# Optimization experiments

Hardware: AMD Instinct MI355X
Metric: run time of the kernel (lower is better)

The kernel has to match this reference:

```python
import jax, jax.numpy as jnp
import numpy as np
from math import sqrt

N = 40000      # nodes
E = 640000     # edges
DIN = 128
H = 128
DOUT = 128
L = 3          # n_layers
TAU = 1.0
MIN_NORM = 1e-15
BN_EPS = 1e-5


def _norm(v):
    return jnp.linalg.norm(v, axis=-1, keepdims=True)


def reflect_at_zero(x, mu):
    # a = reflection_center(mu); isometric_transform(x, a)
    a = mu / jnp.maximum(jnp.sum(mu * mu, -1, keepdims=True), MIN_NORM)
    r2 = jnp.sum(a * a, -1, keepdims=True) - 1.0
    u = x - a
    return r2 / jnp.maximum(jnp.sum(u * u, -1, keepdims=True), MIN_NORM) * u + a


def reflect_through_zero(p, q, x):
    p_ = p / jnp.maximum(_norm(p), MIN_NORM)
    q_ = q / jnp.maximum(_norm(q), MIN_NORM)
    r = q_ - p_
    m = jnp.sum(r * x, -1, keepdims=True) / jnp.sum(r * r, -1, keepdims=True)
    return x - 2.0 * r * m


def logmap0(y):
    yn = jnp.maximum(_norm(y), MIN_NORM)
    return y / yn * jnp.arctanh(jnp.clip(yn, -1.0 + 1e-15, 1.0 - 1e-15))


def gin_layer(x, src, dst, w1, b1, g, bt, w2, b2):
    # GINConv(eps=0, sum aggregation): mlp(x + sum_{j->i} x_j)
    agg = jax.ops.segment_sum(x[src], dst, num_segments=N)  # [N,H]
    h = x + agg
    h = jax.nn.relu(h @ w1.T + b1)
    mu = jnp.mean(h, axis=0)
    var = jnp.mean((h - mu) ** 2, axis=0)  # biased var (BatchNorm training stats)
    h = (h - mu) / jnp.sqrt(var + BN_EPS) * g + bt
    h = jax.nn.relu(h @ w2.T + b2)
    return h


def setup_inputs() -> dict:
    key = jax.random.key(0)
    ks = jax.random.split(key, 16)
    s = 0.05
    x = jax.random.normal(ks[0], (N, DIN), jnp.float32)
    edge_index = jax.random.randint(ks[1], (2, E), 0, N, dtype=jnp.int64)
    fc0_w = jax.random.normal(ks[2], (H, DIN), jnp.float32) * s
    fc0_b = jax.random.normal(ks[3], (H,), jnp.float32) * s
    w1 = jax.random.normal(ks[4], (L, H, H), jnp.float32) * s
    b1 = jax.random.normal(ks[5], (L, H), jnp.float32) * s
    gamma = jnp.ones((L, H), jnp.float32)
    beta = jnp.zeros((L, H), jnp.float32)
    w2 = jax.random.normal(ks[6], (L, H, H), jnp.float32) * s
    b2 = jax.random.normal(ks[7], (L, H), jnp.float32) * s
    fc_out_w = jax.random.normal(ks[8], (DOUT, H), jnp.float32) * s
    fc_out_b = jax.random.normal(ks[9], (DOUT,), jnp.float32) * s
    p = (-1.0 / sqrt(H)) * jnp.ones((H,), jnp.float32)
    return {"x": x, "edge_index": edge_index, "fc0_w": fc0_w, "fc0_b": fc0_b,
            "w1": w1, "b1": b1, "gamma": gamma, "beta": beta, "w2": w2, "b2": b2,
            "fc_out_w": fc_out_w, "fc_out_b": fc_out_b, "p": p}


def reference(x, edge_index, fc0_w, fc0_b, w1, b1, gamma, beta, w2, b2, fc_out_w, fc_out_b, p):
    # With continuous random features every row is unique, so torch.unique(dim=0)
    # is a pure permutation (counts==1) and the unique/scatter_add/gather pipeline
    # collapses to per-node tree embeddings; the final index_select undoes the perm.
    scaling = jnp.tanh(jnp.asarray(TAU, jnp.float32) / 2.0)
    src, dst = edge_index[0], edge_index[1]
    h = jax.nn.relu(x @ fc0_w.T + fc0_b)                 # [N,H]
    hd = jax.lax.stop_gradient(h)                        # unique under no_grad
    z_prev = jnp.zeros((N, H), h.dtype)                  # level-0 root embedding
    z_cur = scaling * hd / _norm(hd)                     # level-1 embedding
    for i in range(L):
        h = gin_layer(h, src, dst, w1[i], b1[i], gamma[i], beta[i], w2[i], b2[i])
        hd = jax.lax.stop_gradient(h)
        z_ch = scaling * hd / _norm(hd)
        z_par = reflect_at_zero(z_prev, z_cur)
        z_ch = reflect_through_zero(z_par, p, z_ch)
        z_all = reflect_at_zero(z_ch, z_cur)
        z_prev, z_cur = z_cur, z_all
    xh = logmap0(z_cur)                                  # [N,H] tangent space
    out = xh @ fc_out_w.T + fc_out_b                     # [N,DOUT]
    return out / jnp.maximum(_norm(out), 1e-12)          # F.normalize
```

## Files before the change

### kernel.cpp

```cpp
#include <hip/hip_runtime.h>
#include <math.h>

#define NN 40000
#define HD 128
#define NE 640000
#define MINN 1e-15f
#define NSB 157
#define GB  2500
#define HB_BLK 512

typedef __attribute__((ext_vector_type(8))) short bf16x8;
typedef __attribute__((ext_vector_type(4))) float f32x4;

__device__ __forceinline__ float red16(float v){
  v += __shfl_xor(v, 1, 64); v += __shfl_xor(v, 2, 64);
  v += __shfl_xor(v, 4, 64); v += __shfl_xor(v, 8, 64);
  return v;
}

__device__ __forceinline__ float bf2f(short h){
  return __uint_as_float(((unsigned)(unsigned short)h) << 16);
}
__device__ __forceinline__ short f2bf(float v){
  unsigned u = __float_as_uint(v);
  u += 0x7FFF + ((u >> 16) & 1);
  return (short)(u >> 16);
}

#define GACC(A,V) \
  A[0] += __uint_as_float((V).x << 16); A[1] += __uint_as_float((V).x & 0xffff0000u); \
  A[2] += __uint_as_float((V).y << 16); A[3] += __uint_as_float((V).y & 0xffff0000u); \
  A[4] += __uint_as_float((V).z << 16); A[5] += __uint_as_float((V).z & 0xffff0000u); \
  A[6] += __uint_as_float((V).w << 16); A[7] += __uint_as_float((V).w & 0xffff0000u);

__device__ __forceinline__ void loadA_g(const float* __restrict__ A, long rb,
                                        int l15, int kg, float av[4][8]){
  #pragma unroll
  for (int ks = 0; ks < 4; ++ks){
    const float* ap = A + (rb + l15)*HD + ks*32 + kg*8;
    float4 a0 = *(const float4*)ap;
    float4 a1 = *(const float4*)(ap + 4);
    av[ks][0]=a0.x; av[ks][1]=a0.y; av[ks][2]=a0.z; av[ks][3]=a0.w;
    av[ks][4]=a1.x; av[ks][5]=a1.y; av[ks][6]=a1.z; av[ks][7]=a1.w;
  }
}

__device__ __forceinline__ void mfma_core(const float av[4][8],
    const bf16x8* __restrict__ bh, const bf16x8* __restrict__ bl,
    int lane, f32x4 acc[8]){
  #pragma unroll
  for (int ct = 0; ct < 8; ++ct){
    acc[ct][0]=0.f; acc[ct][1]=0.f; acc[ct][2]=0.f; acc[ct][3]=0.f;
  }
  #pragma unroll
  for (int ks = 0; ks < 4; ++ks){
    bf16x8 ah, al;
    #pragma unroll
    for (int j = 0; j < 8; ++j){
      float v = av[ks][j];
      short hh = f2bf(v);
      short ll = f2bf(v - bf2f(hh));
      ah[j] = hh; al[j] = ll;
    }
    #pragma unroll
    for (int ct = 0; ct < 8; ++ct){
      bf16x8 bhv = bh[(ks*8 + ct)*64 + lane];
      bf16x8 blv = bl[(ks*8 + ct)*64 + lane];
      acc[ct] = __builtin_amdgcn_mfma_f32_16x16x32_bf16(ah, bhv, acc[ct], 0, 0, 0);
      acc[ct] = __builtin_amdgcn_mfma_f32_16x16x32_bf16(al, bhv, acc[ct], 0, 0, 0);
      acc[ct] = __builtin_amdgcn_mfma_f32_16x16x32_bf16(ah, blv, acc[ct], 0, 0, 0);
    }
  }
}

__device__ __forceinline__ void biasrelu(f32x4 acc[8], const float* __restrict__ bias,
                                         int l15, bool relu){
  #pragma unroll
  for (int ct = 0; ct < 8; ++ct){
    float bb = bias[ct*16 + l15];
    #pragma unroll
    for (int q = 0; q < 4; ++q){
      float v = acc[ct][q] + bb;
      if (relu) v = fmaxf(v, 0.f);
      acc[ct][q] = v;
    }
  }
}

__global__ __launch_bounds__(64) void zero_prep_k(const float* __restrict__ fc0_w,
    const float* __restrict__ w1, const float* __restrict__ w2,
    const float* __restrict__ fco_w, bf16x8* __restrict__ bhi,
    bf16x8* __restrict__ blo, int* __restrict__ cnt, float* __restrict__ part2){
  int bid = blockIdx.x;
  if (bid < 256){
    int gid = bid*64 + threadIdx.x;
    int widx = gid >> 11;
    const float* W;
    if (widx == 0)      W = fc0_w;
    else if (widx <= 3) W = w1 + (size_t)(widx-1)*HD*HD;
    else if (widx <= 6) W = w2 + (size_t)(widx-4)*HD*HD;
    else                W = fco_w;
    int f  = gid & 2047;
    int ln = f & 63;
    int ct = (f >> 6) & 7;
    int ks = f >> 9;
    int n  = ct*16 + (ln & 15);
    int k0 = ks*32 + (ln >> 4)*8;
    bf16x8 hv, lv;
    #pragma unroll
    for (int j = 0; j < 8; ++j){
      float v = W[n*HD + k0 + j];
      short hh = f2bf(v);
      short ll = f2bf(v - bf2f(hh));
      hv[j] = hh; lv[j] = ll;
    }
    bhi[widx*2048 + f] = hv; blo[widx*2048 + f] = lv;
  } else {
    int i = (bid-256)*64 + threadIdx.x;
    const int st = 161*64;
    for (int j = i; j < NN; j += st) cnt[j] = 0;
    for (int j = i; j < 3*2048; j += st) part2[j] = 0.f;
  }
}

__global__ __launch_bounds__(64) void fc0hist_k(const float* __restrict__ x,
    const int* __restrict__ dst, int* __restrict__ cnt,
    const bf16x8* __restrict__ bhi, const bf16x8* __restrict__ blo,
    const float* __restrict__ fc0_b, float* __restrict__ h,
    unsigned short* __restrict__ hb, float* __restrict__ zB, float scaling){
  int bid = blockIdx.x;
  if (bid >= GB){
    int i = (bid - GB)*64 + threadIdx.x;
    const int st = HB_BLK*64;
    for (; i < NE; i += st) atomicAdd(&cnt[dst[i]], 1);
    return;
  }
  const int lane = threadIdx.x;
  const int l15 = lane & 15, kg = lane >> 4;
  const long rb = (long)bid*16;
  float av[4][8]; loadA_g(x, rb, l15, kg, av);
  f32x4 acc[8]; mfma_core(av, bhi, blo, lane, acc);
  biasrelu(acc, fc0_b, l15, true);
  #pragma unroll
  for (int ct = 0; ct < 8; ++ct)
    #pragma unroll
    for (int q = 0; q < 4; ++q){
      float v = acc[ct][q];
      long row = rb + kg*4 + q;
      h[row*HD + ct*16 + l15] = v;
      hb[row*HD + ct*16 + l15] = (unsigned short)f2bf(v);
    }
  #pragma unroll
  for (int q = 0; q < 4; ++q){
    float ss = 0.f;
    #pragma unroll
    for (int ct = 0; ct < 8; ++ct) ss = fmaf(acc[ct][q], acc[ct][q], ss);
    ss = red16(ss);
    float sc2 = scaling / sqrtf(ss);
    long row = rb + kg*4 + q;
    #pragma unroll
    for (int ct = 0; ct < 8; ++ct)
      zB[row*HD + ct*16 + l15] = acc[ct][q]*sc2;
  }
}

__global__ __launch_bounds__(256) void scanall_k(const int* __restrict__ cnt,
    int* __restrict__ ptr, int* __restrict__ fil){
  __shared__ int s[256];
  const int b = blockIdx.x, t = threadIdx.x;
  const int lim = b*256;
  int acc = 0;
  for (int i = t; i < lim; i += 256) acc += cnt[i];
  s[t] = acc; __syncthreads();
  for (int off = 128; off; off >>= 1){
    if (t < off) s[t] += s[t+off];
    __syncthreads();
  }
  const int pre = s[0];
  __syncthreads();
  const int idx = lim + t;
  int v = (idx < NN) ? cnt[idx] : 0;
  s[t] = v; __syncthreads();
  for (int off = 1; off < 256; off <<= 1){
    int x = (t >= off) ? s[t-off] : 0;
    __syncthreads(); s[t] += x; __syncthreads();
  }
  if (idx < NN){
    int v2 = pre + s[t] - v;
    ptr[idx] = v2; fil[idx] = v2;
  }
  if (b == NSB-1 && t == 255) ptr[NN] = pre + s[255];
}

__global__ void fill_k(const int* __restrict__ src, const int* __restrict__ dst,
    int* __restrict__ fill, unsigned short* __restrict__ eidx, int ne){
  int i = blockIdx.x*blockDim.x + threadIdx.x;
  int st = gridDim.x*blockDim.x;
  for (; i < ne; i += st){
    int d = dst[i];
    int pos = atomicAdd(&fill[d], 1);
    eidx[pos] = (unsigned short)src[i];
  }
}

__global__ __launch_bounds__(256) void gw1_k(const float* __restrict__ h,
    const bf16x8* __restrict__ bhi, const bf16x8* __restrict__ blo,
    const float* __restrict__ bias, float* __restrict__ t,
    float* __restrict__ part2, const uint4* __restrict__ hb4,
    const int* __restrict__ gptr, const unsigned short* __restrict__ eidx)
{
  __shared__ float tl[16*132];
  const int tid = threadIdx.x;
  const int lane = tid & 63;
  const int wv = tid >> 6;
  const int l15 = lane & 15, kg = lane >> 4;
  const long rb = (long)blockIdx.x*16;

  {
    const int r = wv*4 + kg;
    const long node = rb + r;
    int beg = gptr[node], end = gptr[node+1];
    const float4* selfp = (const float4*)(h + node*HD) + l15*2;
    float4 s0 = selfp[0], s1 = selfp[1];
    float ga[8] = {s0.x,s0.y,s0.z,s0.w,s1.x,s1.y,s1.z,s1.w};
    int e = beg;
    for (; e + 8 <= end; e += 8){
      int i0 = eidx[e],   i1 = eidx[e+1], i2 = eidx[e+2], i3 = eidx[e+3];
      int i4 = eidx[e+4], i5 = eidx[e+5], i6 = eidx[e+6], i7 = eidx[e+7];
      uint4 v0 = hb4[(long)i0*16 + l15];
      uint4 v1 = hb4[(long)i1*16 + l15];
      uint4 v2 = hb4[(long)i2*16 + l15];
      uint4 v3 = hb4[(long)i3*16 + l15];
      uint4 v4 = hb4[(long)i4*16 + l15];
      uint4 v5 = hb4[(long)i5*16 + l15];
      uint4 v6 = hb4[(long)i6*16 + l15];
      uint4 v7 = hb4[(long)i7*16 + l15];
      GACC(ga,v0) GACC(ga,v1) GACC(ga,v2) GACC(ga,v3)
      GACC(ga,v4) GACC(ga,v5) GACC(ga,v6) GACC(ga,v7)
    }
    if (e + 4 <= end){
      int i0 = eidx[e], i1 = eidx[e+1], i2 = eidx[e+2], i3 = eidx[e+3];
      uint4 v0 = hb4[(long)i0*16 + l15];
      uint4 v1 = hb4[(long)i1*16 + l15];
      uint4 v2 = hb4[(long)i2*16 + l15];
      uint4 v3 = hb4[(long)i3*16 + l15];
      GACC(ga,v0) GACC(ga,v1) GACC(ga,v2) GACC(ga,v3)
      e += 4;
    }
    for (; e < end; ++e){
      uint4 v = hb4[(long)eidx[e]*16 + l15];
      GACC(ga,v)
    }
    float4* tp = (float4*)(tl + r*132 + l15*8);
    float4 o0 = {ga[0],ga[1],ga[2],ga[3]};
    float4 o1 = {ga[4],ga[5],ga[6],ga[7]};
    tp[0] = o0; tp[1] = o1;
  }
  __syncthreads();
  if (wv != 0) return;

  float av[4][8];
  #pragma unroll
  for (int ks = 0; ks < 4; ++ks){
    const float* ap = tl + l15*132 + ks*32 + kg*8;
    float4 a0 = *(const float4*)ap;
    float4 a1 = *(const float4*)(ap + 4);
    av[ks][0]=a0.x; av[ks][1]=a0.y; av[ks][2]=a0.z; av[ks][3]=a0.w;
    av[ks][4]=a1.x; av[ks][5]=a1.y; av[ks][6]=a1.z; av[ks][7]=a1.w;
  }
  f32x4 acc[8]; mfma_core(av, bhi, blo, lane, acc);
  biasrelu(acc, bias, l15, true);

  #pragma unroll
  for (int ct = 0; ct < 8; ++ct){
    float s = 0.f, q2 = 0.f;
    #pragma unroll
    for (int q = 0; q < 4; ++q){
      float v = acc[ct][q];
      s += v; q2 = fmaf(v, v, q2);
    }
    s  += __shfl_xor(s, 16, 64);  s  += __shfl_xor(s, 32, 64);
    q2 += __shfl_xor(q2, 16, 64); q2 += __shfl_xor(q2, 32, 64);
    if (kg == 0){
      const int slot = (blockIdx.x & 7)*256;
      atomicAdd(&part2[slot + ct*16 + l15], s);
      atomicAdd(&part2[slot + 128 + ct*16 + l15], q2);
    }
  }

  #pragma unroll
  for (int ct = 0; ct < 8; ++ct)
    #pragma unroll
    for (int q = 0; q < 4; ++q)
      t[(rb + kg*4 + q)*HD + ct*16 + l15] = acc[ct][q];
}

template<bool WRITE_H, bool ZFIRST>
__global__ __launch_bounds__(64) void w2z_k(const float* __restrict__ A,
    const bf16x8* __restrict__ bhi, const bf16x8* __restrict__ blo,
    const float* __restrict__ bias, const float* __restrict__ part2,
    const float* __restrict__ gam, const float* __restrict__ bet,
    float* __restrict__ hout, unsigned short* __restrict__ hbout,
    float* __restrict__ zout, float scaling,
    const float* __restrict__ zpin, const float* __restrict__ zcin,
    const float* __restrict__ pvec)
{
  __shared__ float bns[256];
  const int lane = threadIdx.x;
  const int l15 = lane & 15, kg = lane >> 4;
  const long rb = (long)blockIdx.x*16;

  #pragma unroll
  for (int h2 = 0; h2 < 2; ++h2){
    const int c = lane + h2*64;
    float s = 0.f, q = 0.f;
    #pragma unroll
    for (int r = 0; r < 8; ++r){
      s += part2[r*256 + c];
      q += part2[r*256 + 128 + c];
    }
    float mu  = s * (1.0f/NN);
    float var = q * (1.0f/NN) - mu*mu;
    float istd = rsqrtf(var + 1e-5f);
    float scv = gam[c]*istd;
    bns[c] = scv;
    bns[128 + c] = fmaf(-mu, scv, bet[c]);
  }

  float av[4][8];
  loadA_g(A, rb, l15, kg, av);

  float zc_a[4][8], zp_a[4][8], pvr[8];
  #pragma unroll
  for (int q = 0; q < 4; ++q){
    const long row = rb + kg*4 + q;
    #pragma unroll
    for (int ct = 0; ct < 8; ++ct)
      zc_a[q][ct] = zcin[row*HD + ct*16 + l15];
  }
  if constexpr (!ZFIRST){
    #pragma unroll
    for (int q = 0; q < 4; ++q){
      const long row = rb + kg*4 + q;
      #pragma unroll
      for (int ct = 0; ct < 8; ++ct)
        zp_a[q][ct] = zpin[row*HD + ct*16 + l15];
    }
  }
  #pragma unroll
  for (int ct = 0; ct < 8; ++ct) pvr[ct] = pvec[ct*16 + l15];

  #pragma unroll
  for (int ks = 0; ks < 4; ++ks){
    const int k0 = ks*32 + kg*8;
    #pragma unroll
    for (int j = 0; j < 8; ++j)
      av[ks][j] = fmaf(av[ks][j], bns[k0 + j], bns[128 + k0 + j]);
  }

  f32x4 acc[8];
  mfma_core(av, bhi, blo, lane, acc);
  biasrelu(acc, bias, l15, true);

  if (WRITE_H){
    #pragma unroll
    for (int ct = 0; ct < 8; ++ct)
      #pragma unroll
      for (int q = 0; q < 4; ++q){
        float v = acc[ct][q];
        long row = rb + kg*4 + q;
        hout[row*HD + ct*16 + l15] = v;
        hbout[row*HD + ct*16 + l15] = (unsigned short)f2bf(v);
      }
  }

  float pq = 0.f;
  #pragma unroll
  for (int ct = 0; ct < 8; ++ct) pq = fmaf(pvr[ct], pvr[ct], pq);
  pq = red16(pq);
  float qi = 1.0f / fmaxf(sqrtf(pq), MINN);
  #pragma unroll
  for (int ct = 0; ct < 8; ++ct) pvr[ct] *= qi;

  #pragma unroll
  for (int q = 0; q < 4; ++q){
    const long row = rb + kg*4 + q;
    float zc[8], zp[8];
    #pragma unroll
    for (int ct = 0; ct < 8; ++ct) zc[ct] = zc_a[q][ct];
    if constexpr (!ZFIRST){
      #pragma unroll
      for (int ct = 0; ct < 8; ++ct) zp[ct] = zp_a[q][ct];
    } else {
      #pragma unroll
      for (int ct = 0; ct < 8; ++ct) zp[ct] = 0.f;
    }
    float hh = 0.f, cc = 0.f;
    #pragma unroll
    for (int ct = 0; ct < 8; ++ct){
      hh = fmaf(acc[ct][q], acc[ct][q], hh);
      cc = fmaf(zc[ct], zc[ct], cc);
    }
    hh = red16(hh); cc = red16(cc);
    float zs = scaling / sqrtf(hh);
    float di = 1.0f / fmaxf(cc, MINN);
    float r2 = cc*di*di - 1.0f;
    float a[8], u[8]; float uu = 0.f;
    #pragma unroll
    for (int ct = 0; ct < 8; ++ct){
      a[ct] = zc[ct]*di;
      u[ct] = zp[ct] - a[ct];
      uu = fmaf(u[ct], u[ct], uu);
    }
    uu = red16(uu);
    float f = r2 / fmaxf(uu, MINN);
    float zpar[8]; float pn2 = 0.f;
    #pragma unroll
    for (int ct = 0; ct < 8; ++ct){
      zpar[ct] = fmaf(f, u[ct], a[ct]);
      pn2 = fmaf(zpar[ct], zpar[ct], pn2);
    }
    pn2 = red16(pn2);
    float pinv = 1.0f / fmaxf(sqrtf(pn2), MINN);
    float rv[8], zch[8]; float rz = 0.f, rr = 0.f;
    #pragma unroll
    for (int ct = 0; ct < 8; ++ct){
      zch[ct] = acc[ct][q]*zs;
      rv[ct] = pvr[ct] - zpar[ct]*pinv;
      rz = fmaf(rv[ct], zch[ct], rz);
      rr = fmaf(rv[ct], rv[ct], rr);
    }
    rz = red16(rz); rr = red16(rr);
    float mm = rz / rr;
    float u2[8]; float uu2 = 0.f;
    #pragma unroll
    for (int ct = 0; ct < 8; ++ct){
      float z2 = fmaf(-2.0f*mm, rv[ct], zch[ct]);
      u2[ct] = z2 - a[ct];
      uu2 = fmaf(u2[ct], u2[ct], uu2);
    }
    uu2 = red16(uu2);
    float f2 = r2 / fmaxf(uu2, MINN);
    #pragma unroll
    for (int ct = 0; ct < 8; ++ct)
      zout[row*HD + ct*16 + l15] = fmaf(f2, u2[ct], a[ct]);
  }
}

__global__ __launch_bounds__(64) void fin_k(const float* __restrict__ A,
    const bf16x8* __restrict__ bhi, const bf16x8* __restrict__ blo,
    const float* __restrict__ bias, float* __restrict__ out)
{
  const int lane = threadIdx.x;
  const int l15 = lane & 15, kg = lane >> 4;
  const long rb = (long)blockIdx.x*16;

  float av[4][8];
  loadA_g(A, rb, l15, kg, av);

  float ss = 0.f;
  #pragma unroll
  for (int ks = 0; ks < 4; ++ks)
    #pragma unroll
    for (int j = 0; j < 8; ++j)
      ss = fmaf(av[ks][j], av[ks][j], ss);
  ss += __shfl_xor(ss, 16, 64);
  ss += __shfl_xor(ss, 32, 64);
  float n = sqrtf(ss);
  float yn = fmaxf(n, MINN);
  float c = fminf(yn, 1.0f);
  float at = 0.5f*logf((1.0f + c)/(1.0f - c));
  float scx = at / yn;
  #pragma unroll
  for (int ks = 0; ks < 4; ++ks)
    #pragma unroll
    for (int j = 0; j < 8; ++j)
      av[ks][j] *= scx;

  f32x4 acc[8];
  mfma_core(av, bhi, blo, lane, acc);
  biasrelu(acc, bias, l15, false);

  float ss4[4] = {0.f,0.f,0.f,0.f};
  #pragma unroll
  for (int ct = 0; ct < 8; ++ct)
    #pragma unroll
    for (int q = 0; q < 4; ++q)
      ss4[q] = fmaf(acc[ct][q], acc[ct][q], ss4[q]);
  #pragma unroll
  for (int q = 0; q < 4; ++q){
    #pragma unroll
    for (int m = 1; m < 16; m <<= 1) ss4[q] += __shfl_xor(ss4[q], m, 64);
    ss4[q] = 1.0f / fmaxf(sqrtf(ss4[q]), 1e-12f);
  }
  #pragma unroll
  for (int ct = 0; ct < 8; ++ct)
    #pragma unroll
    for (int q = 0; q < 4; ++q)
      out[(rb + kg*4 + q)*HD + ct*16 + l15] = acc[ct][q]*ss4[q];
}

extern "C" void kernel_launch(void* const* d_in, const int* in_sizes, int n_in,
                              void* d_out, int out_size, void* d_ws, size_t ws_size,
                              hipStream_t stream) {
  const float* x       = (const float*)d_in[0];
  const int*   ei      = (const int*)  d_in[1];
  const float* fc0_w   = (const float*)d_in[2];
  const float* fc0_b   = (const float*)d_in[3];
  const float* w1      = (const float*)d_in[4];
  const float* b1      = (const float*)d_in[5];
  const float* gamma   = (const float*)d_in[6];
  const float* beta    = (const float*)d_in[7];
  const float* w2      = (const float*)d_in[8];
  const float* b2      = (const float*)d_in[9];
  const float* fco_w   = (const float*)d_in[10];
  const float* fco_b   = (const float*)d_in[11];
  const float* p       = (const float*)d_in[12];

  float* out = (float*)d_out;
  float* ws  = (float*)d_ws;

  float* h     = ws;
  float* zA    = h   + (size_t)NN*HD;
  float* zB    = zA  + (size_t)NN*HD;
  float* part2 = zB  + (size_t)NN*HD;
  bf16x8* bhi  = (bf16x8*)(part2 + 3*2048);
  bf16x8* blo  = bhi + 8*2048;
  unsigned short* hb = (unsigned short*)(blo + 8*2048);
  int* cnt     = (int*)(hb + (size_t)NN*HD);
  int* ptr     = cnt + NN;
  int* fil     = ptr + NN + 1;
  unsigned short* eidx = (unsigned short*)(fil + NN);
  float* t = out;

  const int* src = ei;
  const int* dst = ei + NE;
  const float scaling = tanhf(0.5f);

  zero_prep_k<<<417, 64, 0, stream>>>(fc0_w, w1, w2, fco_w, bhi, blo, cnt, part2);

  fc0hist_k<<<GB + HB_BLK, 64, 0, stream>>>(x, dst, cnt, bhi, blo, fc0_b,
                                            h, hb, zB, scaling);

  scanall_k<<<NSB, 256, 0, stream>>>(cnt, ptr, fil);
  fill_k<<<512, 256, 0, stream>>>(src, dst, fil, eidx, NE);

  float* zprev = zA; float* zcur = zB;

  for (int i = 0; i < 3; ++i) {
    gw1_k<<<GB, 256, 0, stream>>>(
        h, bhi + (1+i)*2048, blo + (1+i)*2048, b1 + i*HD, t, part2 + i*2048,
        (const uint4*)hb, ptr, eidx);
    if (i == 0)
      w2z_k<true,true><<<GB, 64, 0, stream>>>(
          t, bhi + 4*2048, blo + 4*2048, b2, part2, gamma, beta, h, hb,
          zprev, scaling, zprev, zcur, p);
    else if (i == 1)
      w2z_k<true,false><<<GB, 64, 0, stream>>>(
          t, bhi + 5*2048, blo + 5*2048, b2 + HD, part2 + 2048,
          gamma + HD, beta + HD, h, hb, zprev, scaling, zprev, zcur, p);
    else
      w2z_k<false,false><<<GB, 64, 0, stream>>>(
          t, bhi + 6*2048, blo + 6*2048, b2 + 2*HD, part2 + 2*2048,
          gamma + 2*HD, beta + 2*HD, nullptr, nullptr,
          zprev, scaling, zprev, zcur, p);
    float* tmp = zprev; zprev = zcur; zcur = tmp;
  }

  fin_k<<<GB, 64, 0, stream>>>(zcur, bhi + 7*2048, blo + 7*2048, fco_b, out);
}
```

Before: 321.6 us.

## Defer z-step into next layer's gather kernel and precompute BN scale/shift once

Splits the fused W2+z kernel. The W2 pass now only writes h, and the hyperbolic z-update for each layer runs as extra blocks appended to the next layer's gather/W1 launch, so that z work overlaps with the gather. BatchNorm statistics are finalised once in a tiny single-block kernel instead of being reduced again by every block. This adds a re-read of h for the z-step and extra tiny launches, and the in-place zA/zB aliasing needs care.

Result: slower. 336.6 us (+4.7%).

```diff
diff --git a/kernel.cpp b/kernel.cpp
--- a/kernel.cpp
+++ b/kernel.cpp
@@ -7,6 +7,7 @@
 #define MINN 1e-15f
 #define NSB 157
 #define GB  2500
+#define ZSB 625
 #define HB_BLK 512
 
 typedef __attribute__((ext_vector_type(8))) short bf16x8;
@@ -84,6 +85,87 @@
       if (relu) v = fmaxf(v, 0.f);
       acc[ct][q] = v;
     }
+  }
+}
+
+template<bool ZFIRST>
+__device__ __forceinline__ void zstep_tile(const float hv[4][8],
+    const float* __restrict__ zpin, const float* __restrict__ zcin,
+    float* __restrict__ zout, const float* __restrict__ pvec,
+    float scaling, long rb, int l15, int kg){
+  float pvr[8]; float pq = 0.f;
+  #pragma unroll
+  for (int ct = 0; ct < 8; ++ct){
+    float tv = pvec[ct*16 + l15];
+    pvr[ct] = tv; pq = fmaf(tv, tv, pq);
+  }
+  pq = red16(pq);
+  float qi = 1.0f / fmaxf(sqrtf(pq), MINN);
+  #pragma unroll
+  for (int ct = 0; ct < 8; ++ct) pvr[ct] *= qi;
+
+  #pragma unroll
+  for (int q = 0; q < 4; ++q){
+    const long row = rb + kg*4 + q;
+    float zc[8], zp[8];
+    #pragma unroll
+    for (int ct = 0; ct < 8; ++ct) zc[ct] = zcin[row*HD + ct*16 + l15];
+    if constexpr (!ZFIRST){
+      #pragma unroll
+      for (int ct = 0; ct < 8; ++ct) zp[ct] = zpin[row*HD + ct*16 + l15];
+    } else {
+      #pragma unroll
+      for (int ct = 0; ct < 8; ++ct) zp[ct] = 0.f;
+    }
+    float hh = 0.f, cc = 0.f;
+    #pragma unroll
+    for (int ct = 0; ct < 8; ++ct){
+      hh = fmaf(hv[q][ct], hv[q][ct], hh);
+      cc = fmaf(zc[ct], zc[ct], cc);
+    }
+    hh = red16(hh); cc = red16(cc);
+    float zs = scaling / sqrtf(hh);
+    float di = 1.0f / fmaxf(cc, MINN);
+    float r2 = cc*di*di - 1.0f;
+    float a[8], u[8]; float uu = 0.f;
+    #pragma unroll
+    for (int ct = 0; ct < 8; ++ct){
+      a[ct] = zc[ct]*di;
+      u[ct] = zp[ct] - a[ct];
+      uu = fmaf(u[ct], u[ct], uu);
+    }
+    uu = red16(uu);
+    float f = r2 / fmaxf(uu, MINN);
+    float zpar[8]; float pn2 = 0.f;
+    #pragma unroll
+    for (int ct = 0; ct < 8; ++ct){
+      zpar[ct] = fmaf(f, u[ct], a[ct]);
+      pn2 = fmaf(zpar[ct], zpar[ct], pn2);
+    }
+    pn2 = red16(pn2);
+    float pinv = 1.0f / fmaxf(sqrtf(pn2), MINN);
+    float rv[8], zch[8]; float rz = 0.f, rr = 0.f;
+    #pragma unroll
+    for (int ct = 0; ct < 8; ++ct){
+      zch[ct] = hv[q][ct]*zs;
+      rv[ct] = pvr[ct] - zpar[ct]*pinv;
+      rz = fmaf(rv[ct], zch[ct], rz);
+      rr = fmaf(rv[ct], rv[ct], rr);
+    }
+    rz = red16(rz); rr = red16(rr);
+    float mm = rz / rr;
+    float u2[8]; float uu2 = 0.f;
+    #pragma unroll
+    for (int ct = 0; ct < 8; ++ct){
+      float z2 = fmaf(-2.0f*mm, rv[ct], zch[ct]);
+      u2[ct] = z2 - a[ct];
+      uu2 = fmaf(u2[ct], u2[ct], uu2);
+    }
+    uu2 = red16(uu2);
+    float f2 = r2 / fmaxf(uu2, MINN);
+    #pragma unroll
+    for (int ct = 0; ct < 8; ++ct)
+      zout[row*HD + ct*16 + l15] = fmaf(f2, u2[ct], a[ct]);
   }
 }
 
@@ -203,17 +285,36 @@
   }
 }
 
+template<bool ZS, bool ZF>
 __global__ __launch_bounds__(256) void gw1_k(const float* __restrict__ h,
     const bf16x8* __restrict__ bhi, const bf16x8* __restrict__ blo,
     const float* __restrict__ bias, float* __restrict__ t,
     float* __restrict__ part2, const uint4* __restrict__ hb4,
-    const int* __restrict__ gptr, const unsigned short* __restrict__ eidx)
+    const int* __restrict__ gptr, const unsigned short* __restrict__ eidx,
+    const float* __restrict__ zpin, const float* __restrict__ zcin,
+    float* __restrict__ zout, const float* __restrict__ pvec, float scaling)
 {
   __shared__ float tl[16*132];
   const int tid = threadIdx.x;
   const int lane = tid & 63;
   const int wv = tid >> 6;
   const int l15 = lane & 15, kg = lane >> 4;
+
+  if (ZS && blockIdx.x >= GB){
+    const int zt = (blockIdx.x - GB)*4 + wv;
+    const long rb = (long)zt*16;
+    float hv[4][8];
+    #pragma unroll
+    for (int q = 0; q < 4; ++q){
+      const long row = rb + kg*4 + q;
+      #pragma unroll
+      for (int ct = 0; ct < 8; ++ct)
+        hv[q][ct] = h[row*HD + ct*16 + l15];
+    }
+    zstep_tile<ZF>(hv, zpin, zcin, zout, pvec, scaling, rb, l15, kg);
+    return;
+  }
+
   const long rb = (long)blockIdx.x*16;
 
   {
@@ -295,106 +396,124 @@
       t[(rb + kg*4 + q)*HD + ct*16 + l15] = acc[ct][q];
 }
 
-template<bool WRITE_H, bool ZFIRST>
-__global__ __launch_bounds__(64) void w2z_k(const float* __restrict__ A,
+__global__ __launch_bounds__(256) void bnfin_k(const float* __restrict__ part2,
+    const float* __restrict__ g, const float* __restrict__ b,
+    float* __restrict__ scale, float* __restrict__ shift){
+  __shared__ float sm[256];
+  float tot = 0.f;
+  #pragma unroll
+  for (int r = 0; r < 8; ++r) tot += part2[r*256 + threadIdx.x];
+  sm[threadIdx.x] = tot;
+  __syncthreads();
+  if (threadIdx.x < 128){
+    int c = threadIdx.x;
+    float s = sm[c], q = sm[c + 128];
+    float mu  = s * (1.0f/NN);
+    float var = q * (1.0f/NN) - mu*mu;
+    float istd = rsqrtf(var + 1e-5f);
+    float scv = g[c]*istd;
+    scale[c] = scv;
+    shift[c] = fmaf(-mu, scv, b[c]);
+  }
+}
+
+__global__ __launch_bounds__(64) void w2g_k(const float* __restrict__ A,
     const bf16x8* __restrict__ bhi, const bf16x8* __restrict__ blo,
-    const float* __restrict__ bias, const float* __restrict__ part2,
-    const float* __restrict__ gam, const float* __restrict__ bet,
-    float* __restrict__ hout, unsigned short* __restrict__ hbout,
-    float* __restrict__ zout, float scaling,
+    const float* __restrict__ bias, const float* __restrict__ scale,
+    const float* __restrict__ shift, float* __restrict__ hout,
+    unsigned short* __restrict__ hbout)
+{
+  const int lane = threadIdx.x;
+  const int l15 = lane & 15, kg = lane >> 4;
+  const long rb = (long)blockIdx.x*16;
+
+  float av[4][8];
+  loadA_g(A, rb, l15, kg, av);
+  #pragma unroll
+  for (int ks = 0; ks < 4; ++ks){
+    const int k0 = ks*32 + kg*8;
+    float4 s0 = *(const float4*)(scale + k0);
+    float4 s1 = *(const float4*)(scale + k0 + 4);
+    float4 h0 = *(const float4*)(shift + k0);
+    float4 h1 = *(const float4*)(shift + k0 + 4);
+    float sc[8] = {s0.x,s0.y,s0.z,s0.w,s1.x,s1.y,s1.z,s1.w};
+    float sh[8] = {h0.x,h0.y,h0.z,h0.w,h1.x,h1.y,h1.z,h1.w};
+    #pragma unroll
+    for (int j = 0; j < 8; ++j)
+      av[ks][j] = fmaf(av[ks][j], sc[j], sh[j]);
+  }
+  f32x4 acc[8];
+  mfma_core(av, bhi, blo, lane, acc);
+  biasrelu(acc, bias, l15, true);
+  #pragma unroll
+  for (int ct = 0; ct < 8; ++ct)
+    #pragma unroll
+    for (int q = 0; q < 4; ++q){
+      float v = acc[ct][q];
+      long row = rb + kg*4 + q;
+      hout[row*HD + ct*16 + l15] = v;
+      hbout[row*HD + ct*16 + l15] = (unsigned short)f2bf(v);
+    }
+}
+
+__global__ __launch_bounds__(64) void w2z2_k(const float* __restrict__ A,
+    const bf16x8* __restrict__ bhi, const bf16x8* __restrict__ blo,
+    const float* __restrict__ bias, const float* __restrict__ scale,
+    const float* __restrict__ shift, float* __restrict__ zout, float scaling,
     const float* __restrict__ zpin, const float* __restrict__ zcin,
     const float* __restrict__ pvec)
 {
-  __shared__ float bns[256];
   const int lane = threadIdx.x;
   const int l15 = lane & 15, kg = lane >> 4;
   const long rb = (long)blockIdx.x*16;
 
-  #pragma unroll
-  for (int h2 = 0; h2 < 2; ++h2){
-    const int c = lane + h2*64;
-    float s = 0.f, q = 0.f;
-    #pragma unroll
-    for (int r = 0; r < 8; ++r){
-      s += part2[r*256 + c];
-      q += part2[r*256 + 128 + c];
-    }
-    float mu  = s * (1.0f/NN);
-    float var = q * (1.0f/NN) - mu*mu;
-    float istd = rsqrtf(var + 1e-5f);
-    float scv = gam[c]*istd;
-    bns[c] = scv;
-    bns[128 + c] = fmaf(-mu, scv, bet[c]);
-  }
-
   float av[4][8];
   loadA_g(A, rb, l15, kg, av);
 
-  float zc_a[4][8], zp_a[4][8], pvr[8];
+  float zc_a[4][8], zp_a[4][8], pvr8[8];
   #pragma unroll
   for (int q = 0; q < 4; ++q){
     const long row = rb + kg*4 + q;
     #pragma unroll
-    for (int ct = 0; ct < 8; ++ct)
+    for (int ct = 0; ct < 8; ++ct){
       zc_a[q][ct] = zcin[row*HD + ct*16 + l15];
-  }
-  if constexpr (!ZFIRST){
-    #pragma unroll
-    for (int q = 0; q < 4; ++q){
-      const long row = rb + kg*4 + q;
-      #pragma unroll
-      for (int ct = 0; ct < 8; ++ct)
-        zp_a[q][ct] = zpin[row*HD + ct*16 + l15];
-    }
-  }
-  #pragma unroll
-  for (int ct = 0; ct < 8; ++ct) pvr[ct] = pvec[ct*16 + l15];
+      zp_a[q][ct] = zpin[row*HD + ct*16 + l15];
+    }
+  }
+  #pragma unroll
+  for (int ct = 0; ct < 8; ++ct) pvr8[ct] = pvec[ct*16 + l15];
 
   #pragma unroll
   for (int ks = 0; ks < 4; ++ks){
     const int k0 = ks*32 + kg*8;
+    float4 s0 = *(const float4*)(scale + k0);
+    float4 s1 = *(const float4*)(scale + k0 + 4);
+    float4 h0 = *(const float4*)(shift + k0);
+    float4 h1 = *(const float4*)(shift + k0 + 4);
+    float sc[8] = {s0.x,s0.y,s0.z,s0.w,s1.x,s1.y,s1.z,s1.w};
+    float sh[8] = {h0.x,h0.y,h0.z,h0.w,h1.x,h1.y,h1.z,h1.w};
     #pragma unroll
     for (int j = 0; j < 8; ++j)
-      av[ks][j] = fmaf(av[ks][j], bns[k0 + j], bns[128 + k0 + j]);
-  }
-
+      av[ks][j] = fmaf(av[ks][j], sc[j], sh[j]);
+  }
   f32x4 acc[8];
   mfma_core(av, bhi, blo, lane, acc);
   biasrelu(acc, bias, l15, true);
 
-  if (WRITE_H){
-    #pragma unroll
-    for (int ct = 0; ct < 8; ++ct)
-      #pragma unroll
-      for (int q = 0; q < 4; ++q){
-        float v = acc[ct][q];
-        long row = rb + kg*4 + q;
-        hout[row*HD + ct*16 + l15] = v;
-        hbout[row*HD + ct*16 + l15] = (unsigned short)f2bf(v);
-      }
-  }
-
   float pq = 0.f;
   #pragma unroll
-  for (int ct = 0; ct < 8; ++ct) pq = fmaf(pvr[ct], pvr[ct], pq);
+  for (int ct = 0; ct < 8; ++ct) pq = fmaf(pvr8[ct], pvr8[ct], pq);
   pq = red16(pq);
   float qi = 1.0f / fmaxf(sqrtf(pq), MINN);
   #pragma unroll
-  for (int ct = 0; ct < 8; ++ct) pvr[ct] *= qi;
+  for (int ct = 0; ct < 8; ++ct) pvr8[ct] *= qi;
 
   #pragma unroll
   for (int q = 0; q < 4; ++q){
     const long row = rb + kg*4 + q;
     float zc[8], zp[8];
     #pragma unroll
-    for (int ct = 0; ct < 8; ++ct) zc[ct] = zc_a[q][ct];
-    if constexpr (!ZFIRST){
-      #pragma unroll
-      for (int ct = 0; ct < 8; ++ct) zp[ct] = zp_a[q][ct];
-    } else {
-      #pragma unroll
-      for (int ct = 0; ct < 8; ++ct) zp[ct] = 0.f;
-    }
+    for (int ct = 0; ct < 8; ++ct){ zc[ct] = zc_a[q][ct]; zp[ct] = zp_a[q][ct]; }
     float hh = 0.f, cc = 0.f;
     #pragma unroll
     for (int ct = 0; ct < 8; ++ct){
@@ -426,7 +545,7 @@
     #pragma unroll
     for (int ct = 0; ct < 8; ++ct){
       zch[ct] = acc[ct][q]*zs;
-      rv[ct] = pvr[ct] - zpar[ct]*pinv;
+      rv[ct] = pvr8[ct] - zpar[ct]*pinv;
       rz = fmaf(rv[ct], zch[ct], rz);
       rr = fmaf(rv[ct], rv[ct], rr);
     }
@@ -524,7 +643,9 @@
   float* zA    = h   + (size_t)NN*HD;
   float* zB    = zA  + (size_t)NN*HD;
   float* part2 = zB  + (size_t)NN*HD;
-  bf16x8* bhi  = (bf16x8*)(part2 + 3*2048);
+  float* scale = part2 + 3*2048;
+  float* shift = scale + 128;
+  bf16x8* bhi  = (bf16x8*)(shift + 128);
   bf16x8* blo  = bhi + 8*2048;
   unsigned short* hb = (unsigned short*)(blo + 8*2048);
   int* cnt     = (int*)(hb + (size_t)NN*HD);
@@ -545,27 +666,27 @@
   scanall_k<<<NSB, 256, 0, stream>>>(cnt, ptr, fil);
   fill_k<<<512, 256, 0, stream>>>(src, dst, fil, eidx, NE);
 
-  float* zprev = zA; float* zcur = zB;
-
-  for (int i = 0; i < 3; ++i) {
-    gw1_k<<<GB, 256, 0, stream>>>(
-        h, bhi + (1+i)*2048, blo + (1+i)*2048, b1 + i*HD, t, part2 + i*2048,
-        (const uint4*)hb, ptr, eidx);
-    if (i == 0)
-      w2z_k<true,true><<<GB, 64, 0, stream>>>(
-          t, bhi + 4*2048, blo + 4*2048, b2, part2, gamma, beta, h, hb,
-          zprev, scaling, zprev, zcur, p);
-    else if (i == 1)
-      w2z_k<true,false><<<GB, 64, 0, stream>>>(
-          t, bhi + 5*2048, blo + 5*2048, b2 + HD, part2 + 2048,
-          gamma + HD, beta + HD, h, hb, zprev, scaling, zprev, zcur, p);
-    else
-      w2z_k<false,false><<<GB, 64, 0, stream>>>(
-          t, bhi + 6*2048, blo + 6*2048, b2 + 2*HD, part2 + 2*2048,
-          gamma + 2*HD, beta + 2*HD, nullptr, nullptr,
-          zprev, scaling, zprev, zcur, p);
-    float* tmp = zprev; zprev = zcur; zcur = tmp;
-  }
-
-  fin_k<<<GB, 64, 0, stream>>>(zcur, bhi + 7*2048, blo + 7*2048, fco_b, out);
-}
+  gw1_k<false,false><<<GB, 256, 0, stream>>>(
+      h, bhi + 1*2048, blo + 1*2048, b1, t, part2,
+      (const uint4*)hb, ptr, eidx, nullptr, nullptr, nullptr, nullptr, 0.f);
+  bnfin_k<<<1, 256, 0, stream>>>(part2, gamma, beta, scale, shift);
+  w2g_k<<<GB, 64, 0, stream>>>(t, bhi + 4*2048, blo + 4*2048, b2,
+                               scale, shift, h, hb);
+
+  gw1_k<true,true><<<GB + ZSB, 256, 0, stream>>>(
+      h, bhi + 2*2048, blo + 2*2048, b1 + HD, t, part2 + 2048,
+      (const uint4*)hb, ptr, eidx, nullptr, zB, zA, p, scaling);
+  bnfin_k<<<1, 256, 0, stream>>>(part2 + 2048, gamma + HD, beta + HD, scale, shift);
+  w2g_k<<<GB, 64, 0, stream>>>(t, bhi + 5*2048, blo + 5*2048, b2 + HD,
+                               scale, shift, h, hb);
+
+  gw1_k<true,false><<<GB + ZSB, 256, 0, stream>>>(
+      h, bhi + 3*2048, blo + 3*2048, b1 + 2*HD, t, part2 + 2*2048,
+      (const uint4*)hb, ptr, eidx, zB, zA, zB, p, scaling);
+  bnfin_k<<<1, 256, 0, stream>>>(part2 + 2*2048, gamma + 2*HD, beta + 2*HD,
+                                 scale, shift);
+  w2z2_k<<<GB, 64, 0, stream>>>(t, bhi + 6*2048, blo + 6*2048, b2 + 2*HD,
+                                scale, shift, zA, scaling, zA, zB, p);
+
+  fin_k<<<GB, 64, 0, stream>>>(zA, bhi + 7*2048, blo + 7*2048, fco_b, out);
+}
```
